# Performance work log

Measured on AMD Instinct MI355X. Metric: run time of the kernel, lower is better.

Reference implementation:

```python
import jax, jax.numpy as jnp
import numpy as np
import math

N_EMBD = 1024
N_HEAD = 16
HEAD_DIM = N_EMBD // N_HEAD


def setup_inputs() -> dict:
    key = jax.random.key(0)
    ks = jax.random.split(key, 9)
    B, T, E = 4, 2048, N_EMBD
    s = 0.02
    inp = {
        "x": jax.random.normal(ks[0], (B, T, E), dtype=jnp.float32),
        "Wq": jax.random.normal(ks[1], (E, E), dtype=jnp.float32) * s,
        "bq": jnp.zeros((E,), dtype=jnp.float32),
        "Wk": jax.random.normal(ks[2], (E, E), dtype=jnp.float32) * s,
        "bk": jnp.zeros((E,), dtype=jnp.float32),
        "Wv": jax.random.normal(ks[3], (E, E), dtype=jnp.float32) * s,
        "bv": jnp.zeros((E,), dtype=jnp.float32),
        "Wo": jax.random.normal(ks[4], (E, E), dtype=jnp.float32) * s,
        "bo": jnp.zeros((E,), dtype=jnp.float32),
    }
    return inp


def reference(x, Wq, bq, Wk, bk, Wv, bv, Wo, bo):
    B, T, E = x.shape
    H, D = N_HEAD, HEAD_DIM
    # Linear projections (torch Linear: y = x @ W.T + b)
    Q = (x @ Wq.T + bq).reshape(B, T, H, D).transpose(0, 2, 1, 3)  # [B,H,T,D]
    K = (x @ Wk.T + bk).reshape(B, T, H, D).transpose(0, 2, 1, 3)
    V = (x @ Wv.T + bv).reshape(B, T, H, D).transpose(0, 2, 1, 3)
    scale = 1.0 / math.sqrt(D)
    scores = jnp.einsum("bhqd,bhkd->bhqk", Q, K) * scale  # [B,H,T,T]
    causal = jnp.tril(jnp.ones((T, T), dtype=bool))
    scores = jnp.where(causal, scores, jnp.float32(-jnp.inf))
    probs = jax.nn.softmax(scores, axis=-1)
    out = jnp.einsum("bhqk,bhkd->bhqd", probs, V)  # [B,H,T,D]
    out = out.transpose(0, 2, 1, 3).reshape(B, T, E)
    return out @ Wo.T + bo
```

## Files before the change

### kernel.cpp

```cpp
#include <hip/hip_runtime.h>
#include <math.h>


typedef __bf16 bf16x8 __attribute__((ext_vector_type(8)));
typedef float f32x4 __attribute__((ext_vector_type(4)));
typedef unsigned int u32x4 __attribute__((ext_vector_type(4)));
typedef unsigned int uint;
typedef unsigned short ushort;

#define B_ 4
#define T_ 2048
#define E_ 1024
#define H_ 16
#define D_ 64
#define BT_ (B_ * T_)

__device__ __forceinline__ f32x4 mfma16(bf16x8 a, bf16x8 b, f32x4 c) {
  return __builtin_amdgcn_mfma_f32_16x16x32_bf16(a, b, c, 0, 0, 0);
}

__device__ __forceinline__ void gl_lds16(void* lds, const void* g) {
  __builtin_amdgcn_global_load_lds(
      (__attribute__((address_space(1))) unsigned int*)g,
      (__attribute__((address_space(3))) unsigned int*)lds, 16, 0, 0);
}

__device__ __forceinline__ uint pkbf(float a, float b) {
  ushort ux = __builtin_bit_cast(ushort, (__bf16)a);
  ushort uy = __builtin_bit_cast(ushort, (__bf16)b);
  return (uint)ux | ((uint)uy << 16);
}

__global__ __launch_bounds__(256) void cvt_bf16(const float* __restrict__ in,
                                                __bf16* __restrict__ out, int n) {
  int i = (blockIdx.x * 256 + threadIdx.x) * 8;
  if (i >= n) return;
  float4 a = *(const float4*)&in[i];
  float4 b = *(const float4*)&in[i + 4];
  bf16x8 o;
  o[0] = (__bf16)a.x; o[1] = (__bf16)a.y; o[2] = (__bf16)a.z; o[3] = (__bf16)a.w;
  o[4] = (__bf16)b.x; o[5] = (__bf16)b.y; o[6] = (__bf16)b.z; o[7] = (__bf16)b.w;
  *(bf16x8*)&out[i] = o;
}

template <int MODE>
__global__ __launch_bounds__(256) void gemm_nt(const __bf16* __restrict__ A,
                                               const __bf16* __restrict__ Bm,
                                               const float* __restrict__ bias,
                                               void* __restrict__ out,
                                               int M, int N, int K) {
  __shared__ __bf16 sA[128 * 32];
  __shared__ __bf16 sB[128 * 32];
  const int tid = threadIdx.x;
  const int lane = tid & 63;
  const int wv = tid >> 6;
  const int wr = (wv >> 1) << 6;
  const int wc = (wv & 1) << 6;
  const int fr = lane & 15;
  const int fo = (lane >> 4) << 3;
  const int g = lane >> 4;
  const int m0 = blockIdx.y * 128;
  const int n0 = blockIdx.x * 128;

  f32x4 acc[4][4] = {};

  const __bf16* aRow = A + (size_t)(m0 + (tid >> 2)) * K + ((tid & 3) << 3);
  const __bf16* bRow = Bm + (size_t)(n0 + (tid >> 2)) * K + ((tid & 3) << 3);

  for (int kt = 0; kt < K; kt += 32) {
    gl_lds16(&sA[(size_t)tid * 8], aRow + kt);
    gl_lds16(&sA[(size_t)(256 + tid) * 8], aRow + (size_t)64 * K + kt);
    gl_lds16(&sB[(size_t)tid * 8], bRow + kt);
    gl_lds16(&sB[(size_t)(256 + tid) * 8], bRow + (size_t)64 * K + kt);
    __syncthreads();
    bf16x8 af[4], bq[4];
#pragma unroll
    for (int i = 0; i < 4; i++) af[i] = *(const bf16x8*)&sA[(wr + i * 16 + fr) * 32 + fo];
#pragma unroll
    for (int i = 0; i < 4; i++) bq[i] = *(const bf16x8*)&sB[(wc + i * 16 + fr) * 32 + fo];
#pragma unroll
    for (int i = 0; i < 4; i++)
#pragma unroll
      for (int j = 0; j < 4; j++) acc[i][j] = mfma16(af[i], bq[j], acc[i][j]);
    __syncthreads();
  }

#pragma unroll
  for (int i = 0; i < 4; i++) {
#pragma unroll
    for (int j = 0; j < 4; j++) {
#pragma unroll
      for (int r = 0; r < 4; r++) {
        const int m = m0 + wr + i * 16 + g * 4 + r;
        const int n = n0 + wc + j * 16 + fr;
        float v = acc[i][j][r];
        if constexpr (MODE == 0) {
          v += bias[n];
          const int b = m >> 11, t = m & (T_ - 1);
          const int h = n >> 6, d = n & 63;
          ((__bf16*)out)[(((size_t)b * H_ + h) * T_ + t) * D_ + d] = (__bf16)v;
        } else if constexpr (MODE == 1) {
          v += bias[m];
          const int b = n >> 11, t = n & (T_ - 1);
          const int h = m >> 6, d = m & 63;
          ((__bf16*)out)[(((size_t)b * H_ + h) * D_ + d) * T_ + t] = (__bf16)v;
        } else {
          v += bias[n];
          ((float*)out)[(size_t)m * N + n] = v;
        }
      }
    }
  }
}

__global__ __launch_bounds__(256) void attn_fwd(const __bf16* __restrict__ Q,
                                                const __bf16* __restrict__ Kg,
                                                const __bf16* __restrict__ Vt,
                                                __bf16* __restrict__ O) {
  __shared__ __bf16 sK[2][64 * 64];
  __shared__ __bf16 sV[2][64 * 64];
  const int tid = threadIdx.x;
  const int lane = tid & 63;
  const int wv = tid >> 6;
  const int fr = lane & 15;
  const int g = lane >> 4;
  const int k = blockIdx.x;
  const int bh = (k & 7) | ((k >> 6) << 3);
  const int pr = (k >> 3) & 7;
  const __bf16* Qp = Q + (size_t)bh * T_ * D_;
  const __bf16* Kp = Kg + (size_t)bh * T_ * D_;
  const __bf16* Vp = Vt + (size_t)bh * D_ * T_;
  const float SCL = 0.125f * 1.44269504088896f;
  const int addrA = (fr + 32 * (g & 1)) * 4;
  const int swz = fr & 7;
  const int b = bh >> 4, h = bh & 15;

  auto stage = [&](int buf, int kv0) {
#pragma unroll
    for (int rr = 0; rr < 2; ++rr) {
      const int idx = rr * 256 + tid;
      const int row = idx >> 3, ch = idx & 7;
      gl_lds16(&sK[buf][idx * 8],
               Kp + (size_t)(kv0 + row) * D_ + ((ch ^ (row & 7)) << 3));
      gl_lds16(&sV[buf][idx * 8],
               Vp + (size_t)row * T_ + kv0 + ((ch ^ (row & 7)) << 3));
    }
  };

#pragma unroll 1
  for (int pass = 0; pass < 2; ++pass) {
    const int s = pass ? 15 - pr : pr;
    const int qw = s * 128 + wv * 32;
    const int ntile = 2 * s + 2;

    bf16x8 qf[2][2];
#pragma unroll
    for (int mf = 0; mf < 2; mf++)
#pragma unroll
      for (int kc = 0; kc < 2; kc++)
        qf[mf][kc] =
            *(const bf16x8*)&Qp[(size_t)(qw + mf * 16 + fr) * D_ + kc * 32 + g * 8];

    f32x4 acc[2][4] = {};
    float mrun[2] = {-INFINITY, -INFINITY};
    float lrun[2] = {0.f, 0.f};

    stage(0, 0);
    __syncthreads();
    int cur = 0;

#pragma unroll 1
    for (int kt = 0; kt < ntile; ++kt) {
      const int kv0 = kt << 6;
      if (kt + 1 < ntile) stage(cur ^ 1, (kt + 1) << 6);

      if (kv0 <= qw + 31) {
        f32x4 st[4][2] = {};
        __builtin_amdgcn_s_setprio(1);
#pragma unroll
        for (int kvf = 0; kvf < 4; ++kvf) {
          const int row = kvf * 16 + fr;
          bf16x8 kf0 = *(const bf16x8*)&sK[cur][row * 64 + ((g ^ swz) << 3)];
          bf16x8 kf1 = *(const bf16x8*)&sK[cur][row * 64 + (((g + 4) ^ swz) << 3)];
#pragma unroll
          for (int mf = 0; mf < 2; ++mf) {
            st[kvf][mf] = mfma16(kf0, qf[mf][0], st[kvf][mf]);
            st[kvf][mf] = mfma16(kf1, qf[mf][1], st[kvf][mf]);
          }
        }
        __builtin_amdgcn_s_setprio(0);

        if (kv0 + 63 > qw) {
#pragma unroll
          for (int kvf = 0; kvf < 4; ++kvf)
#pragma unroll
            for (int mf = 0; mf < 2; ++mf)
#pragma unroll
              for (int r = 0; r < 4; ++r)
                if (kv0 + kvf * 16 + g * 4 + r > qw + mf * 16 + fr)
                  st[kvf][mf][r] = -INFINITY;
        }

        uint W[2][2][4];
#pragma unroll
        for (int mf = 0; mf < 2; ++mf) {
          float rm[4];
#pragma unroll
          for (int kvf = 0; kvf < 4; ++kvf)
            rm[kvf] = fmaxf(fmaxf(st[kvf][mf][0], st[kvf][mf][1]),
                            fmaxf(st[kvf][mf][2], st[kvf][mf][3]));
          float rmax = fmaxf(fmaxf(rm[0], rm[1]), fmaxf(rm[2], rm[3])) * SCL;

          if (!__all(rmax - mrun[mf] <= 8.f)) {
            float rfull = fmaxf(rmax, __shfl_xor(rmax, 16, 64));
            rfull = fmaxf(rfull, __shfl_xor(rfull, 32, 64));
            const float mn = fmaxf(mrun[mf], rfull);
            const float corr = exp2f(mrun[mf] - mn);
            mrun[mf] = mn;
            lrun[mf] *= corr;
            float cg[4];
#pragma unroll
            for (int r = 0; r < 4; ++r) cg[r] = __shfl(corr, g * 4 + r, 64);
#pragma unroll
            for (int nd = 0; nd < 4; ++nd)
#pragma unroll
              for (int r = 0; r < 4; ++r) acc[mf][nd][r] *= cg[r];
          }

          float p[4][4];
          float ls = 0.f;
#pragma unroll
          for (int kvf = 0; kvf < 4; ++kvf)
#pragma unroll
            for (int r = 0; r < 4; ++r) {
              p[kvf][r] = exp2f(fmaf(st[kvf][mf][r], SCL, -mrun[mf]));
              ls += p[kvf][r];
            }
          lrun[mf] += ls;

          uint w[4][2];
#pragma unroll
          for (int kvf = 0; kvf < 4; ++kvf) {
            w[kvf][0] = pkbf(p[kvf][0], p[kvf][1]);
            w[kvf][1] = pkbf(p[kvf][2], p[kvf][3]);
          }
#pragma unroll
          for (int kc = 0; kc < 2; ++kc)
#pragma unroll
            for (int m = 0; m < 4; ++m) {
              const int a = addrA + (m >> 1) * 64;
              int t0 = __builtin_amdgcn_ds_bpermute(a, (int)w[2 * kc][m & 1]);
              int t1 = __builtin_amdgcn_ds_bpermute(a, (int)w[2 * kc + 1][m & 1]);
              W[mf][kc][m] = (uint)((g >> 1) ? t1 : t0);
            }
        }

        __builtin_amdgcn_s_setprio(1);
#pragma unroll
        for (int kc = 0; kc < 2; ++kc) {
          bf16x8 pa[2];
#pragma unroll
          for (int mf = 0; mf < 2; ++mf) {
            u32x4 t;
            t[0] = W[mf][kc][0]; t[1] = W[mf][kc][1];
            t[2] = W[mf][kc][2]; t[3] = W[mf][kc][3];
            pa[mf] = __builtin_bit_cast(bf16x8, t);
          }
#pragma unroll
          for (int nd = 0; nd < 4; ++nd) {
            const int row = nd * 16 + fr;
            bf16x8 vf =
                *(const bf16x8*)&sV[cur][row * 64 + (((4 * kc + g) ^ swz) << 3)];
#pragma unroll
            for (int mf = 0; mf < 2; ++mf)
              acc[mf][nd] = mfma16(pa[mf], vf, acc[mf][nd]);
          }
        }
        __builtin_amdgcn_s_setprio(0);
      }

      __syncthreads();
      cur ^= 1;
    }

#pragma unroll
    for (int mf = 0; mf < 2; ++mf) {
      lrun[mf] += __shfl_xor(lrun[mf], 16, 64);
      lrun[mf] += __shfl_xor(lrun[mf], 32, 64);
    }
#pragma unroll
    for (int mf = 0; mf < 2; ++mf) {
      float linv[4];
#pragma unroll
      for (int r = 0; r < 4; ++r) linv[r] = 1.f / __shfl(lrun[mf], g * 4 + r, 64);
#pragma unroll
      for (int nd = 0; nd < 4; ++nd)
#pragma unroll
        for (int r = 0; r < 4; ++r) {
          const int t = qw + mf * 16 + g * 4 + r;
          O[(((size_t)b * T_ + t) * H_ + h) * D_ + nd * 16 + fr] =
              (__bf16)(acc[mf][nd][r] * linv[r]);
        }
    }
  }
}

extern "C" void kernel_launch(void* const* d_in, const int* in_sizes, int n_in,
                              void* d_out, int out_size, void* d_ws, size_t ws_size,
                              hipStream_t stream) {
  const float* x  = (const float*)d_in[0];
  const float* Wq = (const float*)d_in[1];
  const float* bq = (const float*)d_in[2];
  const float* Wk = (const float*)d_in[3];
  const float* bk = (const float*)d_in[4];
  const float* Wv = (const float*)d_in[5];
  const float* bv = (const float*)d_in[6];
  const float* Wo = (const float*)d_in[7];
  const float* bo = (const float*)d_in[8];

  char* w = (char*)d_ws;
  __bf16* xb  = (__bf16*)w; w += (size_t)BT_ * E_ * 2;
  __bf16* Wqb = (__bf16*)w; w += (size_t)E_ * E_ * 2;
  __bf16* Wkb = (__bf16*)w; w += (size_t)E_ * E_ * 2;
  __bf16* Wvb = (__bf16*)w; w += (size_t)E_ * E_ * 2;
  __bf16* Wob = (__bf16*)w; w += (size_t)E_ * E_ * 2;
  __bf16* Qb  = (__bf16*)w; w += (size_t)BT_ * E_ * 2;
  __bf16* Kb  = (__bf16*)w; w += (size_t)BT_ * E_ * 2;
  __bf16* Vtb = (__bf16*)w; w += (size_t)BT_ * E_ * 2;
  __bf16* Ob  = (__bf16*)w; w += (size_t)BT_ * E_ * 2;

  cvt_bf16<<<(BT_ * E_) / 2048, 256, 0, stream>>>(x, xb, BT_ * E_);
  cvt_bf16<<<(E_ * E_) / 2048, 256, 0, stream>>>(Wq, Wqb, E_ * E_);
  cvt_bf16<<<(E_ * E_) / 2048, 256, 0, stream>>>(Wk, Wkb, E_ * E_);
  cvt_bf16<<<(E_ * E_) / 2048, 256, 0, stream>>>(Wv, Wvb, E_ * E_);
  cvt_bf16<<<(E_ * E_) / 2048, 256, 0, stream>>>(Wo, Wob, E_ * E_);

  gemm_nt<0><<<dim3(E_ / 128, BT_ / 128), 256, 0, stream>>>(xb, Wqb, bq, Qb, BT_, E_, E_);
  gemm_nt<0><<<dim3(E_ / 128, BT_ / 128), 256, 0, stream>>>(xb, Wkb, bk, Kb, BT_, E_, E_);
  gemm_nt<1><<<dim3(BT_ / 128, E_ / 128), 256, 0, stream>>>(Wvb, xb, bv, Vtb, E_, BT_, E_);

  attn_fwd<<<512, 256, 0, stream>>>(Qb, Kb, Vtb, Ob);

  gemm_nt<2><<<dim3(E_ / 128, BT_ / 128), 256, 0, stream>>>(Ob, Wob, bo, d_out, BT_, E_, E_);
}
```

Before: 238.9 us.

## Batch weight casts and QKV GEMMs into single launches, split attention blocks

Merges the four weight conversion launches into one 2D-grid kernel and the three Q/K/V projection GEMMs into one kernel indexed by blockIdx.z. This removes launch gaps and lets the three GEMMs fill the GPU together. Attention goes from 512 blocks that each handled two balanced query strips to 1024 blocks with one strip each, ordered heaviest-first so the scheduler can balance the load. The trade-off is that each attention block does unequal work and Q fragments and setup are loaded per block rather than reused across two passes.

```diff
diff --git a/kernel.cpp b/kernel.cpp
--- a/kernel.cpp
+++ b/kernel.cpp
@@ -35,6 +35,31 @@
                                                 __bf16* __restrict__ out, int n) {
   int i = (blockIdx.x * 256 + threadIdx.x) * 8;
   if (i >= n) return;
+  float4 a = *(const float4*)&in[i];
+  float4 b = *(const float4*)&in[i + 4];
+  bf16x8 o;
+  o[0] = (__bf16)a.x; o[1] = (__bf16)a.y; o[2] = (__bf16)a.z; o[3] = (__bf16)a.w;
+  o[4] = (__bf16)b.x; o[5] = (__bf16)b.y; o[6] = (__bf16)b.z; o[7] = (__bf16)b.w;
+  *(bf16x8*)&out[i] = o;
+}
+
+__global__ __launch_bounds__(256) void cvt_w4(const float* __restrict__ w0,
+                                              const float* __restrict__ w1,
+                                              const float* __restrict__ w2,
+                                              const float* __restrict__ w3,
+                                              __bf16* __restrict__ o0,
+                                              __bf16* __restrict__ o1,
+                                              __bf16* __restrict__ o2,
+                                              __bf16* __restrict__ o3) {
+  const float* in;
+  __bf16* out;
+  switch (blockIdx.y) {
+    case 0: in = w0; out = o0; break;
+    case 1: in = w1; out = o1; break;
+    case 2: in = w2; out = o2; break;
+    default: in = w3; out = o3; break;
+  }
+  int i = (blockIdx.x * 256 + threadIdx.x) * 8;
   float4 a = *(const float4*)&in[i];
   float4 b = *(const float4*)&in[i + 4];
   bf16x8 o;
@@ -93,20 +118,93 @@
       for (int r = 0; r < 4; r++) {
         const int m = m0 + wr + i * 16 + g * 4 + r;
         const int n = n0 + wc + j * 16 + fr;
+        float v = acc[i][j][r] + bias[n];
+        ((float*)out)[(size_t)m * N + n] = v;
+      }
+    }
+  }
+}
+
+__global__ __launch_bounds__(256) void gemm_qkv(const __bf16* __restrict__ xb,
+                                                const __bf16* __restrict__ Wq,
+                                                const __bf16* __restrict__ Wk,
+                                                const __bf16* __restrict__ Wv,
+                                                const float* __restrict__ bq,
+                                                const float* __restrict__ bk,
+                                                const float* __restrict__ bv,
+                                                __bf16* __restrict__ Qb,
+                                                __bf16* __restrict__ Kb,
+                                                __bf16* __restrict__ Vtb) {
+  __shared__ __bf16 sA[128 * 32];
+  __shared__ __bf16 sB[128 * 32];
+  const int z = blockIdx.z;
+  const __bf16* A;
+  const __bf16* Bm;
+  const float* bias;
+  int m0, n0;
+  if (z == 0) {
+    A = xb; Bm = Wq; bias = bq;
+    m0 = blockIdx.y * 128; n0 = blockIdx.x * 128;
+  } else if (z == 1) {
+    A = xb; Bm = Wk; bias = bk;
+    m0 = blockIdx.y * 128; n0 = blockIdx.x * 128;
+  } else {
+    A = Wv; Bm = xb; bias = bv;
+    m0 = blockIdx.x * 128; n0 = blockIdx.y * 128;
+  }
+  const int K = E_;
+  const int tid = threadIdx.x;
+  const int lane = tid & 63;
+  const int wv = tid >> 6;
+  const int wr = (wv >> 1) << 6;
+  const int wc = (wv & 1) << 6;
+  const int fr = lane & 15;
+  const int fo = (lane >> 4) << 3;
+  const int g = lane >> 4;
+
+  f32x4 acc[4][4] = {};
+
+  const __bf16* aRow = A + (size_t)(m0 + (tid >> 2)) * K + ((tid & 3) << 3);
+  const __bf16* bRow = Bm + (size_t)(n0 + (tid >> 2)) * K + ((tid & 3) << 3);
+
+  for (int kt = 0; kt < K; kt += 32) {
+    gl_lds16(&sA[(size_t)tid * 8], aRow + kt);
+    gl_lds16(&sA[(size_t)(256 + tid) * 8], aRow + (size_t)64 * K + kt);
+    gl_lds16(&sB[(size_t)tid * 8], bRow + kt);
+    gl_lds16(&sB[(size_t)(256 + tid) * 8], bRow + (size_t)64 * K + kt);
+    __syncthreads();
+    bf16x8 af[4], bq4[4];
+#pragma unroll
+    for (int i = 0; i < 4; i++) af[i] = *(const bf16x8*)&sA[(wr + i * 16 + fr) * 32 + fo];
+#pragma unroll
+    for (int i = 0; i < 4; i++) bq4[i] = *(const bf16x8*)&sB[(wc + i * 16 + fr) * 32 + fo];
+#pragma unroll
+    for (int i = 0; i < 4; i++)
+#pragma unroll
+      for (int j = 0; j < 4; j++) acc[i][j] = mfma16(af[i], bq4[j], acc[i][j]);
+    __syncthreads();
+  }
+
+#pragma unroll
+  for (int i = 0; i < 4; i++) {
+#pragma unroll
+    for (int j = 0; j < 4; j++) {
+#pragma unroll
+      for (int r = 0; r < 4; r++) {
+        const int m = m0 + wr + i * 16 + g * 4 + r;
+        const int n = n0 + wc + j * 16 + fr;
         float v = acc[i][j][r];
-        if constexpr (MODE == 0) {
+        if (z == 2) {
+          v += bias[m];
+          const int b = n >> 11, t = n & (T_ - 1);
+          const int h = m >> 6, d = m & 63;
+          Vtb[(((size_t)b * H_ + h) * D_ + d) * T_ + t] = (__bf16)v;
+        } else {
           v += bias[n];
           const int b = m >> 11, t = m & (T_ - 1);
           const int h = n >> 6, d = n & 63;
-          ((__bf16*)out)[(((size_t)b * H_ + h) * T_ + t) * D_ + d] = (__bf16)v;
-        } else if constexpr (MODE == 1) {
-          v += bias[m];
-          const int b = n >> 11, t = n & (T_ - 1);
-          const int h = m >> 6, d = m & 63;
-          ((__bf16*)out)[(((size_t)b * H_ + h) * D_ + d) * T_ + t] = (__bf16)v;
-        } else {
-          v += bias[n];
-          ((float*)out)[(size_t)m * N + n] = v;
+          __bf16* out = (z == 0) ? Qb : Kb;
+          out[(((size_t)b * H_ + h) * T_ + t) * D_ + d] = (__bf16)v;
         }
       }
     }
@@ -125,8 +223,9 @@
   const int fr = lane & 15;
   const int g = lane >> 4;
   const int k = blockIdx.x;
-  const int bh = (k & 7) | ((k >> 6) << 3);
-  const int pr = (k >> 3) & 7;
+  const int j = k >> 3;
+  const int bh = (k & 7) + ((j >> 4) << 3);
+  const int s = 15 - (j & 15);
   const __bf16* Qp = Q + (size_t)bh * T_ * D_;
   const __bf16* Kp = Kg + (size_t)bh * T_ * D_;
   const __bf16* Vp = Vt + (size_t)bh * D_ * T_;
@@ -147,161 +246,157 @@
     }
   };
 
+  const int qw = s * 128 + wv * 32;
+  const int ntile = 2 * s + 2;
+
+  bf16x8 qf[2][2];
+#pragma unroll
+  for (int mf = 0; mf < 2; mf++)
+#pragma unroll
+    for (int kc = 0; kc < 2; kc++)
+      qf[mf][kc] =
+          *(const bf16x8*)&Qp[(size_t)(qw + mf * 16 + fr) * D_ + kc * 32 + g * 8];
+
+  f32x4 acc[2][4] = {};
+  float mrun[2] = {-INFINITY, -INFINITY};
+  float lrun[2] = {0.f, 0.f};
+
+  stage(0, 0);
+  __syncthreads();
+  int cur = 0;
+
 #pragma unroll 1
-  for (int pass = 0; pass < 2; ++pass) {
-    const int s = pass ? 15 - pr : pr;
-    const int qw = s * 128 + wv * 32;
-    const int ntile = 2 * s + 2;
-
-    bf16x8 qf[2][2];
-#pragma unroll
-    for (int mf = 0; mf < 2; mf++)
-#pragma unroll
-      for (int kc = 0; kc < 2; kc++)
-        qf[mf][kc] =
-            *(const bf16x8*)&Qp[(size_t)(qw + mf * 16 + fr) * D_ + kc * 32 + g * 8];
-
-    f32x4 acc[2][4] = {};
-    float mrun[2] = {-INFINITY, -INFINITY};
-    float lrun[2] = {0.f, 0.f};
-
-    stage(0, 0);
+  for (int kt = 0; kt < ntile; ++kt) {
+    const int kv0 = kt << 6;
+    if (kt + 1 < ntile) stage(cur ^ 1, (kt + 1) << 6);
+
+    if (kv0 <= qw + 31) {
+      f32x4 st[4][2] = {};
+      __builtin_amdgcn_s_setprio(1);
+#pragma unroll
+      for (int kvf = 0; kvf < 4; ++kvf) {
+        const int row = kvf * 16 + fr;
+        bf16x8 kf0 = *(const bf16x8*)&sK[cur][row * 64 + ((g ^ swz) << 3)];
+        bf16x8 kf1 = *(const bf16x8*)&sK[cur][row * 64 + (((g + 4) ^ swz) << 3)];
+#pragma unroll
+        for (int mf = 0; mf < 2; ++mf) {
+          st[kvf][mf] = mfma16(kf0, qf[mf][0], st[kvf][mf]);
+          st[kvf][mf] = mfma16(kf1, qf[mf][1], st[kvf][mf]);
+        }
+      }
+      __builtin_amdgcn_s_setprio(0);
+
+      if (kv0 + 63 > qw) {
+#pragma unroll
+        for (int kvf = 0; kvf < 4; ++kvf)
+#pragma unroll
+          for (int mf = 0; mf < 2; ++mf)
+#pragma unroll
+            for (int r = 0; r < 4; ++r)
+              if (kv0 + kvf * 16 + g * 4 + r > qw + mf * 16 + fr)
+                st[kvf][mf][r] = -INFINITY;
+      }
+
+      uint W[2][2][4];
+#pragma unroll
+      for (int mf = 0; mf < 2; ++mf) {
+        float rm[4];
+#pragma unroll
+        for (int kvf = 0; kvf < 4; ++kvf)
+          rm[kvf] = fmaxf(fmaxf(st[kvf][mf][0], st[kvf][mf][1]),
+                          fmaxf(st[kvf][mf][2], st[kvf][mf][3]));
+        float rmax = fmaxf(fmaxf(rm[0], rm[1]), fmaxf(rm[2], rm[3])) * SCL;
+
+        if (!__all(rmax - mrun[mf] <= 8.f)) {
+          float rfull = fmaxf(rmax, __shfl_xor(rmax, 16, 64));
+          rfull = fmaxf(rfull, __shfl_xor(rfull, 32, 64));
+          const float mn = fmaxf(mrun[mf], rfull);
+          const float corr = exp2f(mrun[mf] - mn);
+          mrun[mf] = mn;
+          lrun[mf] *= corr;
+          float cg[4];
+#pragma unroll
+          for (int r = 0; r < 4; ++r) cg[r] = __shfl(corr, g * 4 + r, 64);
+#pragma unroll
+          for (int nd = 0; nd < 4; ++nd)
+#pragma unroll
+            for (int r = 0; r < 4; ++r) acc[mf][nd][r] *= cg[r];
+        }
+
+        float p[4][4];
+        float ls = 0.f;
+#pragma unroll
+        for (int kvf = 0; kvf < 4; ++kvf)
+#pragma unroll
+          for (int r = 0; r < 4; ++r) {
+            p[kvf][r] = exp2f(fmaf(st[kvf][mf][r], SCL, -mrun[mf]));
+            ls += p[kvf][r];
+          }
+        lrun[mf] += ls;
+
+        uint w[4][2];
+#pragma unroll
+        for (int kvf = 0; kvf < 4; ++kvf) {
+          w[kvf][0] = pkbf(p[kvf][0], p[kvf][1]);
+          w[kvf][1] = pkbf(p[kvf][2], p[kvf][3]);
+        }
+#pragma unroll
+        for (int kc = 0; kc < 2; ++kc)
+#pragma unroll
+          for (int m = 0; m < 4; ++m) {
+            const int a = addrA + (m >> 1) * 64;
+            int t0 = __builtin_amdgcn_ds_bpermute(a, (int)w[2 * kc][m & 1]);
+            int t1 = __builtin_amdgcn_ds_bpermute(a, (int)w[2 * kc + 1][m & 1]);
+            W[mf][kc][m] = (uint)((g >> 1) ? t1 : t0);
+          }
+      }
+
+      __builtin_amdgcn_s_setprio(1);
+#pragma unroll
+      for (int kc = 0; kc < 2; ++kc) {
+        bf16x8 pa[2];
+#pragma unroll
+        for (int mf = 0; mf < 2; ++mf) {
+          u32x4 t;
+          t[0] = W[mf][kc][0]; t[1] = W[mf][kc][1];
+          t[2] = W[mf][kc][2]; t[3] = W[mf][kc][3];
+          pa[mf] = __builtin_bit_cast(bf16x8, t);
+        }
+#pragma unroll
+        for (int nd = 0; nd < 4; ++nd) {
+          const int row = nd * 16 + fr;
+          bf16x8 vf =
+              *(const bf16x8*)&sV[cur][row * 64 + (((4 * kc + g) ^ swz) << 3)];
+#pragma unroll
+          for (int mf = 0; mf < 2; ++mf)
+            acc[mf][nd] = mfma16(pa[mf], vf, acc[mf][nd]);
+        }
+      }
+      __builtin_amdgcn_s_setprio(0);
+    }
+
     __syncthreads();
-    int cur = 0;
-
-#pragma unroll 1
-    for (int kt = 0; kt < ntile; ++kt) {
-      const int kv0 = kt << 6;
-      if (kt + 1 < ntile) stage(cur ^ 1, (kt + 1) << 6);
-
-      if (kv0 <= qw + 31) {
-        f32x4 st[4][2] = {};
-        __builtin_amdgcn_s_setprio(1);
-#pragma unroll
-        for (int kvf = 0; kvf < 4; ++kvf) {
-          const int row = kvf * 16 + fr;
-          bf16x8 kf0 = *(const bf16x8*)&sK[cur][row * 64 + ((g ^ swz) << 3)];
-          bf16x8 kf1 = *(const bf16x8*)&sK[cur][row * 64 + (((g + 4) ^ swz) << 3)];
-#pragma unroll
-          for (int mf = 0; mf < 2; ++mf) {
-            st[kvf][mf] = mfma16(kf0, qf[mf][0], st[kvf][mf]);
-            st[kvf][mf] = mfma16(kf1, qf[mf][1], st[kvf][mf]);
-          }
-        }
-        __builtin_amdgcn_s_setprio(0);
-
-        if (kv0 + 63 > qw) {
-#pragma unroll
-          for (int kvf = 0; kvf < 4; ++kvf)
-#pragma unroll
-            for (int mf = 0; mf < 2; ++mf)
-#pragma unroll
-              for (int r = 0; r < 4; ++r)
-                if (kv0 + kvf * 16 + g * 4 + r > qw + mf * 16 + fr)
-                  st[kvf][mf][r] = -INFINITY;
-        }
-
-        uint W[2][2][4];
-#pragma unroll
-        for (int mf = 0; mf < 2; ++mf) {
-          float rm[4];
-#pragma unroll
-          for (int kvf = 0; kvf < 4; ++kvf)
-            rm[kvf] = fmaxf(fmaxf(st[kvf][mf][0], st[kvf][mf][1]),
-                            fmaxf(st[kvf][mf][2], st[kvf][mf][3]));
-          float rmax = fmaxf(fmaxf(rm[0], rm[1]), fmaxf(rm[2], rm[3])) * SCL;
-
-          if (!__all(rmax - mrun[mf] <= 8.f)) {
-            float rfull = fmaxf(rmax, __shfl_xor(rmax, 16, 64));
-            rfull = fmaxf(rfull, __shfl_xor(rfull, 32, 64));
-            const float mn = fmaxf(mrun[mf], rfull);
-            const float corr = exp2f(mrun[mf] - mn);
-            mrun[mf] = mn;
-            lrun[mf] *= corr;
-            float cg[4];
-#pragma unroll
-            for (int r = 0; r < 4; ++r) cg[r] = __shfl(corr, g * 4 + r, 64);
-#pragma unroll
-            for (int nd = 0; nd < 4; ++nd)
-#pragma unroll
-              for (int r = 0; r < 4; ++r) acc[mf][nd][r] *= cg[r];
-          }
-
-          float p[4][4];
-          float ls = 0.f;
-#pragma unroll
-          for (int kvf = 0; kvf < 4; ++kvf)
-#pragma unroll
-            for (int r = 0; r < 4; ++r) {
-              p[kvf][r] = exp2f(fmaf(st[kvf][mf][r], SCL, -mrun[mf]));
-              ls += p[kvf][r];
-            }
-          lrun[mf] += ls;
-
-          uint w[4][2];
-#pragma unroll
-          for (int kvf = 0; kvf < 4; ++kvf) {
-            w[kvf][0] = pkbf(p[kvf][0], p[kvf][1]);
-            w[kvf][1] = pkbf(p[kvf][2], p[kvf][3]);
-          }
-#pragma unroll
-          for (int kc = 0; kc < 2; ++kc)
-#pragma unroll
-            for (int m = 0; m < 4; ++m) {
-              const int a = addrA + (m >> 1) * 64;
-              int t0 = __builtin_amdgcn_ds_bpermute(a, (int)w[2 * kc][m & 1]);
-              int t1 = __builtin_amdgcn_ds_bpermute(a, (int)w[2 * kc + 1][m & 1]);
-              W[mf][kc][m] = (uint)((g >> 1) ? t1 : t0);
-            }
-        }
-
-        __builtin_amdgcn_s_setprio(1);
-#pragma unroll
-        for (int kc = 0; kc < 2; ++kc) {
-          bf16x8 pa[2];
-#pragma unroll
-          for (int mf = 0; mf < 2; ++mf) {
-            u32x4 t;
-            t[0] = W[mf][kc][0]; t[1] = W[mf][kc][1];
-            t[2] = W[mf][kc][2]; t[3] = W[mf][kc][3];
-            pa[mf] = __builtin_bit_cast(bf16x8, t);
-          }
-#pragma unroll
-          for (int nd = 0; nd < 4; ++nd) {
-            const int row = nd * 16 + fr;
-            bf16x8 vf =
-                *(const bf16x8*)&sV[cur][row * 64 + (((4 * kc + g) ^ swz) << 3)];
-#pragma unroll
-            for (int mf = 0; mf < 2; ++mf)
-              acc[mf][nd] = mfma16(pa[mf], vf, acc[mf][nd]);
-          }
-        }
-        __builtin_amdgcn_s_setprio(0);
-      }
-
-      __syncthreads();
-      cur ^= 1;
-    }
-
-#pragma unroll
-    for (int mf = 0; mf < 2; ++mf) {
-      lrun[mf] += __shfl_xor(lrun[mf], 16, 64);
-      lrun[mf] += __shfl_xor(lrun[mf], 32, 64);
-    }
-#pragma unroll
-    for (int mf = 0; mf < 2; ++mf) {
-      float linv[4];
-#pragma unroll
-      for (int r = 0; r < 4; ++r) linv[r] = 1.f / __shfl(lrun[mf], g * 4 + r, 64);
-#pragma unroll
-      for (int nd = 0; nd < 4; ++nd)
-#pragma unroll
-        for (int r = 0; r < 4; ++r) {
-          const int t = qw + mf * 16 + g * 4 + r;
-          O[(((size_t)b * T_ + t) * H_ + h) * D_ + nd * 16 + fr] =
-              (__bf16)(acc[mf][nd][r] * linv[r]);
-        }
-    }
+    cur ^= 1;
+  }
+
+#pragma unroll
+  for (int mf = 0; mf < 2; ++mf) {
+    lrun[mf] += __shfl_xor(lrun[mf], 16, 64);
+    lrun[mf] += __shfl_xor(lrun[mf], 32, 64);
+  }
+#pragma unroll
+  for (int mf = 0; mf < 2; ++mf) {
+    float linv[4];
+#pragma unroll
+    for (int r = 0; r < 4; ++r) linv[r] = 1.f / __shfl(lrun[mf], g * 4 + r, 64);
+#pragma unroll
+    for (int nd = 0; nd < 4; ++nd)
+#pragma unroll
+      for (int r = 0; r < 4; ++r) {
+        const int t = qw + mf * 16 + g * 4 + r;
+        O[(((size_t)b * T_ + t) * H_ + h) * D_ + nd * 16 + fr] =
+            (__bf16)(acc[mf][nd][r] * linv[r]);
+      }
   }
 }
 
@@ -330,16 +425,13 @@
   __bf16* Ob  = (__bf16*)w; w += (size_t)BT_ * E_ * 2;
 
   cvt_bf16<<<(BT_ * E_) / 2048, 256, 0, stream>>>(x, xb, BT_ * E_);
-  cvt_bf16<<<(E_ * E_) / 2048, 256, 0, stream>>>(Wq, Wqb, E_ * E_);
-  cvt_bf16<<<(E_ * E_) / 2048, 256, 0, stream>>>(Wk, Wkb, E_ * E_);
-  cvt_bf16<<<(E_ * E_) / 2048, 256, 0, stream>>>(Wv, Wvb, E_ * E_);
-  cvt_bf16<<<(E_ * E_) / 2048, 256, 0, stream>>>(Wo, Wob, E_ * E_);
-
-  gemm_nt<0><<<dim3(E_ / 128, BT_ / 128), 256, 0, stream>>>(xb, Wqb, bq, Qb, BT_, E_, E_);
-  gemm_nt<0><<<dim3(E_ / 128, BT_ / 128), 256, 0, stream>>>(xb, Wkb, bk, Kb, BT_, E_, E_);
-  gemm_nt<1><<<dim3(BT_ / 128, E_ / 128), 256, 0, stream>>>(Wvb, xb, bv, Vtb, E_, BT_, E_);
-
-  attn_fwd<<<512, 256, 0, stream>>>(Qb, Kb, Vtb, Ob);
+  cvt_w4<<<dim3((E_ * E_) / 2048, 4), 256, 0, stream>>>(Wq, Wk, Wv, Wo,
+                                                        Wqb, Wkb, Wvb, Wob);
+
+  gemm_qkv<<<dim3(E_ / 128, BT_ / 128, 3), 256, 0, stream>>>(
+      xb, Wqb, Wkb, Wvb, bq, bk, bv, Qb, Kb, Vtb);
+
+  attn_fwd<<<1024, 256, 0, stream>>>(Qb, Kb, Vtb, Ob);
 
   gemm_nt<2><<<dim3(E_ / 128, BT_ / 128), 256, 0, stream>>>(Ob, Wob, bo, d_out, BT_, E_, E_);
 }
```

New measurement: 272.9 us. 14.3% more time.
